# Performance work log

Measured on AMD Instinct MI355X. Metric: run time of the kernel, lower is better.

## Reference

```python
import jax, jax.numpy as jnp
import numpy as np

N_EMBEDS = 1024
N_HEADS = 16
HEAD_DIM = N_EMBEDS // N_HEADS
SCALE = HEAD_DIM ** (-0.5)
B, T = 2, 2048


def setup_inputs() -> dict:
    key = jax.random.key(0)
    k1, k2, k3, k4 = jax.random.split(key, 4)
    x = jax.random.normal(k1, (B, T, N_EMBEDS), dtype=jnp.float32)
    # Glorot-uniform-style init like keras Dense defaults (scale irrelevant for correctness)
    w_qkv = jax.random.normal(k2, (N_EMBEDS, 3 * N_EMBEDS), dtype=jnp.float32) * (N_EMBEDS ** -0.5)
    w_proj = jax.random.normal(k3, (N_EMBEDS, N_EMBEDS), dtype=jnp.float32) * (N_EMBEDS ** -0.5)
    b_proj = jnp.zeros((N_EMBEDS,), dtype=jnp.float32)
    return {"x": x, "w_qkv": w_qkv, "w_proj": w_proj, "b_proj": b_proj}


def reference(x, w_qkv, w_proj, b_proj):
    Bc, Tc, D = x.shape
    qkv = x @ w_qkv                                   # [B,T,3D]
    q, k, v = jnp.split(qkv, 3, axis=-1)
    def heads(t):
        return t.reshape(Bc, Tc, N_HEADS, HEAD_DIM).transpose(0, 2, 1, 3)  # [B,H,T,hd]
    q, k, v = heads(q), heads(k), heads(v)
    att = jnp.einsum("bhqd,bhkd->bhqk", q, k) * SCALE  # [B,H,T,T]
    causal = jnp.tril(jnp.ones((Tc, Tc), dtype=bool))[None, None]
    att = jnp.where(causal, att, jnp.float32(-1e9))
    att = jax.nn.softmax(att, axis=-1)
    out = jnp.einsum("bhqk,bhkd->bhqd", att, v)        # [B,H,T,hd]
    out = out.transpose(0, 2, 1, 3).reshape(Bc, Tc, D)
    return out @ w_proj + b_proj
```

## Files before the change

kernel.cpp:

```cpp
#include <hip/hip_runtime.h>
#include <hip/hip_bf16.h>


typedef __bf16 bf16;
typedef float f32x4 __attribute__((ext_vector_type(4)));
typedef float f32x16 __attribute__((ext_vector_type(16)));
typedef bf16 bf16x4 __attribute__((ext_vector_type(4)));
typedef bf16 bf16x8 __attribute__((ext_vector_type(8)));

#define B_ 2
#define T_ 2048
#define D_ 1024
#define H_ 16
#define HD_ 64
#define QSPLIT 9

__device__ __forceinline__ f32x16 mfma32(bf16x8 a, bf16x8 b, f32x16 c) {
    return __builtin_amdgcn_mfma_f32_32x32x16_bf16(a, b, c, 0, 0, 0);
}

__device__ __forceinline__ void gload16(void* l, const void* g) {
    __builtin_amdgcn_global_load_lds(
        (const __attribute__((address_space(1))) unsigned int*)g,
        (__attribute__((address_space(3))) unsigned int*)l, 16, 0, 0);
}

__device__ __forceinline__ f32x16 z16() {
    f32x16 v;
#pragma unroll
    for (int i = 0; i < 16; ++i) v[i] = 0.f;
    return v;
}

__global__ __launch_bounds__(256) void prep(
    const float* __restrict__ x, bf16* __restrict__ xb,
    const float* __restrict__ wqkv, bf16* __restrict__ wqkvt,
    const float* __restrict__ wproj, bf16* __restrict__ wprojt) {
    __shared__ float tile[32][33];
    const int bid = blockIdx.x;
    const int tid = threadIdx.x;
    if (bid < 4096) {
        int i = bid * 256 + tid;
        float4 v = ((const float4*)x)[i];
        bf16x4 o = { (bf16)v.x, (bf16)v.y, (bf16)v.z, (bf16)v.w };
        ((bf16x4*)xb)[i] = o;
        return;
    }
    const float* in;
    bf16* outp;
    int C, bx, by;
    if (bid < 4096 + 3072) {
        int r = bid - 4096;
        in = wqkv; outp = wqkvt; C = 3 * D_; bx = r % 96; by = r / 96;
    } else {
        int r = bid - 7168;
        in = wproj; outp = wprojt; C = D_; bx = r % 32; by = r / 32;
    }
    const int R = D_;
    const int tx = tid & 31, ty = tid >> 5;
    int cx = bx * 32 + tx;
    int r0 = by * 32;
#pragma unroll
    for (int j = 0; j < 32; j += 8)
        tile[ty + j][tx] = in[(size_t)(r0 + ty + j) * C + cx];
    __syncthreads();
    int rx = r0 + tx;
    int c0 = bx * 32;
#pragma unroll
    for (int j = 0; j < 32; j += 8)
        outp[(size_t)(c0 + ty + j) * R + rx] = (bf16)tile[tx][ty + j];
}

template <int MW, int NWN, int EPI>
__global__ __launch_bounds__(256) void gemm_k(
    const bf16* __restrict__ A, const bf16* __restrict__ Bt,
    int M, int N, int K,
    bf16* __restrict__ qb, bf16* __restrict__ kb, bf16* __restrict__ vt,
    const float* __restrict__ bias, float* __restrict__ outf) {
    constexpr int BM = 64 * MW;
    constexpr int BN = 64 * NWN;
    __shared__ bf16 sA[BM * 64];
    __shared__ bf16 sB[BN * 64];
    const int tid = threadIdx.x;
    const int wave = tid >> 6, lane = tid & 63;
    const int ln = lane & 31, hi = lane >> 5;
    const int wr = (wave >> 1) * (32 * MW);
    const int wc = (wave & 1) * (32 * NWN);
    const int m0 = blockIdx.x * BM, n0 = blockIdx.y * BN;

    f32x16 acc[MW][NWN];
#pragma unroll
    for (int mi = 0; mi < MW; ++mi)
#pragma unroll
        for (int ni = 0; ni < NWN; ++ni) acc[mi][ni] = z16();

    for (int k0 = 0; k0 < K; k0 += 64) {
        __syncthreads();
#pragma unroll
        for (int j = 0; j < 2 * MW; ++j) {
            int c = tid + 256 * j;
            int r = c >> 3, g = (c & 7) ^ (r & 7);
            gload16(&sA[c * 8], A + (size_t)(m0 + r) * K + k0 + 8 * g);
        }
#pragma unroll
        for (int j = 0; j < 2 * NWN; ++j) {
            int c = tid + 256 * j;
            int r = c >> 3, g = (c & 7) ^ (r & 7);
            gload16(&sB[c * 8], Bt + (size_t)(n0 + r) * K + k0 + 8 * g);
        }
        __syncthreads();
#pragma unroll
        for (int s = 0; s < 4; ++s) {
            bf16x8 av[MW], bv[NWN];
#pragma unroll
            for (int mi = 0; mi < MW; ++mi) {
                int r = wr + mi * 32 + ln;
                av[mi] = *(const bf16x8*)((const char*)sA + r * 128 +
                                          ((((s << 1) | hi) ^ (r & 7)) << 4));
            }
#pragma unroll
            for (int ni = 0; ni < NWN; ++ni) {
                int r = wc + ni * 32 + ln;
                bv[ni] = *(const bf16x8*)((const char*)sB + r * 128 +
                                          ((((s << 1) | hi) ^ (r & 7)) << 4));
            }
#pragma unroll
            for (int mi = 0; mi < MW; ++mi)
#pragma unroll
                for (int ni = 0; ni < NWN; ++ni)
                    acc[mi][ni] = mfma32(av[mi], bv[ni], acc[mi][ni]);
        }
    }

#pragma unroll
    for (int mi = 0; mi < MW; ++mi)
#pragma unroll
        for (int ni = 0; ni < NWN; ++ni) {
            int col = n0 + wc + ni * 32 + ln;
            if (EPI == 0) {
                int part = col >> 10, h = (col >> 6) & 15, d = col & 63;
                if (part == 2) {
#pragma unroll
                    for (int g4 = 0; g4 < 4; ++g4) {
                        int row = m0 + wr + mi * 32 + 8 * g4 + 4 * hi;
                        int bb = row >> 11, tt = row & (T_ - 1);
                        bf16x4 w;
#pragma unroll
                        for (int j = 0; j < 4; ++j)
                            w[j] = (bf16)acc[mi][ni][4 * g4 + j];
                        *(bf16x4*)&vt[(((size_t)(bb * H_ + h) * HD_) + d) * T_ + tt] = w;
                    }
                } else {
                    bf16* dst = (part == 0) ? qb : kb;
#pragma unroll
                    for (int r = 0; r < 16; ++r) {
                        int row = m0 + wr + mi * 32 + (r & 3) + 8 * (r >> 2) + 4 * hi;
                        int bb = row >> 11, tt = row & (T_ - 1);
                        dst[((size_t)(bb * H_ + h) * T_ + tt) * HD_ + d] =
                            (bf16)acc[mi][ni][r];
                    }
                }
            } else {
#pragma unroll
                for (int r = 0; r < 16; ++r) {
                    int row = m0 + wr + mi * 32 + (r & 3) + 8 * (r >> 2) + 4 * hi;
                    outf[(size_t)row * N + col] = acc[mi][ni][r] + bias[col];
                }
            }
        }
}

static __device__ const signed char QT_T[23] = {
    8, 7, 15, 15, 14, 14, 6, 13, 10, 10, 5, 11, 11, 12, 12, 13,
    0, 1, 2, 3, 4, 9, 9};
static __device__ const signed char SEG_T[23] = {
    -1, -1, 0, 1, 0, 1, -1, 0, 0, 1, -1, 0, 1, 0, 1, 1,
    -1, -1, -1, -1, -1, 0, 1};

__device__ __forceinline__ bf16x8 kread(const char* base, int row, int s, int hi) {
    int b = (row * 128 + s * 32 + hi * 16) ^ ((row & 7) << 4);
    return *(const bf16x8*)(base + b);
}
__device__ __forceinline__ bf16x8 vread(const char* base, int row, int s, int hi) {
    int sw = (row & 7) << 4;
    int b0 = (row * 128 + s * 32 + hi * 8) ^ sw;
    int b1 = (row * 128 + s * 32 + hi * 8 + 16) ^ sw;
    bf16x4 lo = *(const bf16x4*)(base + b0);
    bf16x4 hi4 = *(const bf16x4*)(base + b1);
    return __builtin_shufflevector(lo, hi4, 0, 1, 2, 3, 4, 5, 6, 7);
}

__global__ __launch_bounds__(256, 3) void attn_kernel(
    const bf16* __restrict__ qb, const bf16* __restrict__ kb,
    const bf16* __restrict__ vtb, bf16* __restrict__ ob,
    bf16* __restrict__ oP, float2* __restrict__ mlP) {
    __shared__ bf16 sK2[2][4096];
    __shared__ bf16 sV2[2][4096];

    const int bid = blockIdx.x;
    const int bh = bid & 31;
    const int sid = bid >> 5;
    const int qt = QT_T[sid];
    const int seg = SEG_T[sid];
    int t0, t1;
    if (seg < 0)       { t0 = 0;      t1 = 2 * qt + 2; }
    else if (seg == 0) { t0 = 0;      t1 = qt + 1; }
    else               { t0 = qt + 1; t1 = 2 * qt + 2; }
    const int b = bh >> 4, h = bh & 15;
    const int tid = threadIdx.x, wave = tid >> 6, lane = tid & 63;
    const int ln = lane & 31, hi = lane >> 5;
    const int qs = qt * 128 + wave * 32;
    const int qrow = qs + ln;

    const bf16* Qg = qb + (size_t)bh * (T_ * HD_);
    const bf16* Kg = kb + (size_t)bh * (T_ * HD_);
    const bf16* Vtg = vtb + (size_t)bh * (HD_ * T_);

    bf16x8 qf[4];
#pragma unroll
    for (int s = 0; s < 4; ++s) {
        bf16x8 v = *(const bf16x8*)&Qg[(size_t)qrow * HD_ + s * 16 + hi * 8];
#pragma unroll
        for (int e = 0; e < 8; ++e) v[e] = (bf16)((float)v[e] * 0.1803368801f);
        qf[s] = v;
    }
    bf16x8 ones;
#pragma unroll
    for (int e = 0; e < 8; ++e) ones[e] = (bf16)1.0f;

    const int rr0 = tid >> 3;
    const int gg = ((tid & 7) ^ (rr0 & 7)) * 8;

    {
        int kv0 = t0 * 64;
        gload16(&sK2[0][tid * 8], Kg + (size_t)(kv0 + rr0) * HD_ + gg);
        gload16(&sK2[0][(tid + 256) * 8], Kg + (size_t)(kv0 + rr0 + 32) * HD_ + gg);
        gload16(&sV2[0][tid * 8], Vtg + (size_t)rr0 * T_ + kv0 + gg);
        gload16(&sV2[0][(tid + 256) * 8], Vtg + (size_t)(rr0 + 32) * T_ + kv0 + gg);
    }
    __syncthreads();

    const float NINF = -__builtin_inff();
    f32x16 oA = z16(), oB = z16();
    float mR = NINF, lR = 0.f;
    int cur = 0;

    for (int t = t0; t < t1; ++t) {
        if ((t + 1) < t1) {
            int kv0 = (t + 1) * 64;
            bf16* kd = sK2[cur ^ 1];
            bf16* vd = sV2[cur ^ 1];
            gload16(&kd[tid * 8], Kg + (size_t)(kv0 + rr0) * HD_ + gg);
            gload16(&kd[(tid + 256) * 8], Kg + (size_t)(kv0 + rr0 + 32) * HD_ + gg);
            gload16(&vd[tid * 8], Vtg + (size_t)rr0 * T_ + kv0 + gg);
            gload16(&vd[(tid + 256) * 8], Vtg + (size_t)(rr0 + 32) * T_ + kv0 + gg);
        }

        if (64 * t <= qs + 31) {
            const char* kbase = (const char*)sK2[cur];
            const char* vbase = (const char*)sV2[cur];

            f32x16 p0 = z16(), p1 = z16();
            __builtin_amdgcn_s_setprio(1);
#pragma unroll
            for (int s = 0; s < 4; ++s) {
                bf16x8 a0 = kread(kbase, ln, s, hi);
                bf16x8 a1 = kread(kbase, ln + 32, s, hi);
                p0 = mfma32(a0, qf[s], p0);
                p1 = mfma32(a1, qf[s], p1);
            }
            __builtin_amdgcn_s_setprio(0);

            if (64 * t + 63 > qs) {
                int kvb = 64 * t + 4 * hi;
#pragma unroll
                for (int r = 0; r < 16; ++r) {
                    int kvr = kvb + (r & 3) + 8 * (r >> 2);
                    if (kvr > qrow) p0[r] = NINF;
                    if (kvr + 32 > qrow) p1[r] = NINF;
                }
            }

            float mx0 = NINF, mx1 = NINF, mx2 = NINF, mx3 = NINF;
#pragma unroll
            for (int r = 0; r < 16; r += 4) {
                mx0 = fmaxf(fmaxf(p0[r], p1[r]), mx0);
                mx1 = fmaxf(fmaxf(p0[r + 1], p1[r + 1]), mx1);
                mx2 = fmaxf(fmaxf(p0[r + 2], p1[r + 2]), mx2);
                mx3 = fmaxf(fmaxf(p0[r + 3], p1[r + 3]), mx3);
            }
            float pm = fmaxf(fmaxf(mx0, mx1), fmaxf(mx2, mx3));
            pm = fmaxf(pm, __shfl_xor(pm, 32));

            if (__any(pm > mR + 8.f)) {
                float mnew = fmaxf(mR, pm);
                float fac = exp2f(mR - mnew);
                lR *= fac;
#pragma unroll
                for (int r = 0; r < 16; ++r) { oA[r] *= fac; oB[r] *= fac; }
                mR = mnew;
            }

            bf16x8 pa0, pa1, pa2, pa3;
#pragma unroll
            for (int e = 0; e < 8; ++e) {
                pa0[e] = (bf16)exp2f(p0[e] - mR);
                pa1[e] = (bf16)exp2f(p0[8 + e] - mR);
                pa2[e] = (bf16)exp2f(p1[e] - mR);
                pa3[e] = (bf16)exp2f(p1[8 + e] - mR);
            }

            __builtin_amdgcn_s_setprio(1);
            f32x16 sacc = mfma32(ones, pa0, z16());
            sacc = mfma32(ones, pa1, sacc);
            sacc = mfma32(ones, pa2, sacc);
            sacc = mfma32(ones, pa3, sacc);
#pragma unroll
            for (int s = 0; s < 4; ++s) {
                bf16x8 pas = (s == 0) ? pa0 : (s == 1) ? pa1 : (s == 2) ? pa2 : pa3;
                oA = mfma32(vread(vbase, ln, s, hi), pas, oA);
                oB = mfma32(vread(vbase, ln + 32, s, hi), pas, oB);
            }
            __builtin_amdgcn_s_setprio(0);
            lR += sacc[0];
        }

        __syncthreads();
        cur ^= 1;
    }

    if (seg < 0) {
        float inv = 1.f / lR;
        bf16* orow = ob + ((size_t)(b * T_ + qrow)) * D_ + h * HD_;
#pragma unroll
        for (int g = 0; g < 4; ++g) {
            bf16x4 w, w2;
#pragma unroll
            for (int j = 0; j < 4; ++j) {
                w[j] = (bf16)(oA[4 * g + j] * inv);
                w2[j] = (bf16)(oB[4 * g + j] * inv);
            }
            *(bf16x4*)&orow[4 * hi + 8 * g] = w;
            *(bf16x4*)&orow[32 + 4 * hi + 8 * g] = w2;
        }
    } else {
        int row = wave * 32 + ln;
        bf16* prow;
        if (seg == 0) {
            prow = ob + ((size_t)(b * T_ + qrow)) * D_ + h * HD_;
        } else {
            size_t sbase = (size_t)bh * (16 - QSPLIT) + (qt - QSPLIT);
            prow = oP + (sbase * 128 + row) * 64;
        }
#pragma unroll
        for (int g = 0; g < 4; ++g) {
            bf16x4 w, w2;
#pragma unroll
            for (int j = 0; j < 4; ++j) {
                w[j] = (bf16)oA[4 * g + j];
                w2[j] = (bf16)oB[4 * g + j];
            }
            *(bf16x4*)&prow[4 * hi + 8 * g] = w;
            *(bf16x4*)&prow[32 + 4 * hi + 8 * g] = w2;
        }
        if (hi == 0)
            mlP[(((size_t)bh * (16 - QSPLIT) + (qt - QSPLIT)) * 2 + seg) * 128 + row] =
                make_float2(mR, lR);
    }
}

__global__ __launch_bounds__(256) void attn_merge(
    const bf16* __restrict__ oP, const float2* __restrict__ mlP,
    bf16* __restrict__ ob) {
    constexpr int NQS = 16 - QSPLIT;
    int gid = blockIdx.x * 256 + threadIdx.x;
    int bh = gid / (NQS * 128);
    int rem = gid - bh * (NQS * 128);
    int qi = rem >> 7, row = rem & 127;
    int b = bh >> 4, h = bh & 15;
    int t = (QSPLIT + qi) * 128 + row;
    size_t sbase = (size_t)bh * NQS + qi;
    float2 ml0 = mlP[(sbase * 2 + 0) * 128 + row];
    float2 ml1 = mlP[(sbase * 2 + 1) * 128 + row];
    float ms = fmaxf(ml0.x, ml1.x);
    float w0 = exp2f(ml0.x - ms), w1 = exp2f(ml1.x - ms);
    float inv = 1.f / (ml0.y * w0 + ml1.y * w1);
    w0 *= inv; w1 *= inv;
    bf16* dst = ob + ((size_t)(b * T_ + t)) * D_ + h * HD_;
    const bf16* r1 = oP + (sbase * 128 + row) * 64;
#pragma unroll
    for (int g = 0; g < 8; ++g) {
        bf16x8 a = *(const bf16x8*)&dst[g * 8];
        bf16x8 c = *(const bf16x8*)&r1[g * 8];
        bf16x8 o;
#pragma unroll
        for (int j = 0; j < 8; ++j)
            o[j] = (bf16)((float)a[j] * w0 + (float)c[j] * w1);
        *(bf16x8*)&dst[g * 8] = o;
    }
}

extern "C" void kernel_launch(void* const* d_in, const int* in_sizes, int n_in,
                              void* d_out, int out_size, void* d_ws, size_t ws_size,
                              hipStream_t stream) {
    const float* x = (const float*)d_in[0];
    const float* w_qkv = (const float*)d_in[1];
    const float* w_proj = (const float*)d_in[2];
    const float* b_proj = (const float*)d_in[3];
    float* out = (float*)d_out;
    char* ws = (char*)d_ws;

    bf16* xb = (bf16*)(ws);
    bf16* ob = (bf16*)(ws);
    bf16* wqkvt = (bf16*)(ws + 8388608);
    bf16* oP = (bf16*)(ws + 8388608);
    float2* mlP = (float2*)(ws + 12058624);
    bf16* wprojt = (bf16*)(ws + 14680064);
    bf16* qbuf = (bf16*)(ws + 16777216);
    bf16* kbuf = (bf16*)(ws + 25165824);
    bf16* vtbuf = (bf16*)(ws + 33554432);

    prep<<<8192, 256, 0, stream>>>(x, xb, w_qkv, wqkvt, w_proj, wprojt);

    gemm_k<2, 2, 0><<<dim3((B_ * T_) / 128, (3 * D_) / 128), 256, 0, stream>>>(
        xb, wqkvt, B_ * T_, 3 * D_, D_, qbuf, kbuf, vtbuf, nullptr, nullptr);

    attn_kernel<<<23 * 32, 256, 0, stream>>>(qbuf, kbuf, vtbuf, ob, oP, mlP);
    attn_merge<<<112, 256, 0, stream>>>(oP, mlP, ob);

    gemm_k<1, 2, 1><<<dim3((B_ * T_) / 64, D_ / 128), 256, 0, stream>>>(
        ob, wprojt, B_ * T_, D_, D_, nullptr, nullptr, nullptr, b_proj, out);
}
```

Before: 110.6 us.

## Use 256-row query tiles with 512 threads and up-to-3-way KV split

The attention kernel moves from 128-row query tiles with 256 threads to 256-row tiles with 512 threads (8 waves), so each staged K/V tile is shared by more query rows. A new static schedule splits long causal strips into 2 or 3 KV segments, and the merge kernel combines up to three partials. The w_proj transpose moves from the prep kernel into spare blocks of the merge launch, and workspace buffers are re-laid out to alias the freed K buffer. The aim is more K/V reuse and better load balance across CUs, at the cost of fewer, larger blocks and a more intricate merge.

```diff
diff --git a/kernel.cpp b/kernel.cpp
--- a/kernel.cpp
+++ b/kernel.cpp
@@ -13,7 +13,8 @@
 #define D_ 1024
 #define H_ 16
 #define HD_ 64
-#define QSPLIT 9
+#define SEGS_PER_BH 15
+#define PSLOTS 7
 
 __device__ __forceinline__ f32x16 mfma32(bf16x8 a, bf16x8 b, f32x16 c) {
     return __builtin_amdgcn_mfma_f32_32x32x16_bf16(a, b, c, 0, 0, 0);
@@ -34,8 +35,7 @@
 
 __global__ __launch_bounds__(256) void prep(
     const float* __restrict__ x, bf16* __restrict__ xb,
-    const float* __restrict__ wqkv, bf16* __restrict__ wqkvt,
-    const float* __restrict__ wproj, bf16* __restrict__ wprojt) {
+    const float* __restrict__ wqkv, bf16* __restrict__ wqkvt) {
     __shared__ float tile[32][33];
     const int bid = blockIdx.x;
     const int tid = threadIdx.x;
@@ -46,29 +46,21 @@
         ((bf16x4*)xb)[i] = o;
         return;
     }
-    const float* in;
-    bf16* outp;
-    int C, bx, by;
-    if (bid < 4096 + 3072) {
-        int r = bid - 4096;
-        in = wqkv; outp = wqkvt; C = 3 * D_; bx = r % 96; by = r / 96;
-    } else {
-        int r = bid - 7168;
-        in = wproj; outp = wprojt; C = D_; bx = r % 32; by = r / 32;
-    }
-    const int R = D_;
+    int r = bid - 4096;
+    const int C = 3 * D_;
+    int bx = r % 96, by = r / 96;
     const int tx = tid & 31, ty = tid >> 5;
     int cx = bx * 32 + tx;
     int r0 = by * 32;
 #pragma unroll
     for (int j = 0; j < 32; j += 8)
-        tile[ty + j][tx] = in[(size_t)(r0 + ty + j) * C + cx];
+        tile[ty + j][tx] = wqkv[(size_t)(r0 + ty + j) * C + cx];
     __syncthreads();
     int rx = r0 + tx;
     int c0 = bx * 32;
 #pragma unroll
     for (int j = 0; j < 32; j += 8)
-        outp[(size_t)(c0 + ty + j) * R + rx] = (bf16)tile[tx][ty + j];
+        wqkvt[(size_t)(c0 + ty + j) * D_ + rx] = (bf16)tile[tx][ty + j];
 }
 
 template <int MW, int NWN, int EPI>
@@ -170,12 +162,14 @@
         }
 }
 
-static __device__ const signed char QT_T[23] = {
-    8, 7, 15, 15, 14, 14, 6, 13, 10, 10, 5, 11, 11, 12, 12, 13,
-    0, 1, 2, 3, 4, 9, 9};
-static __device__ const signed char SEG_T[23] = {
-    -1, -1, 0, 1, 0, 1, -1, 0, 0, 1, -1, 0, 1, 0, 1, 1,
-    -1, -1, -1, -1, -1, 0, 1};
+static __device__ const signed char QT_T[SEGS_PER_BH] =
+    {5, 5, 2, 7, 7, 7, 6, 6, 4, 4, 6, 3, 3, 1, 0};
+static __device__ const signed char SEG_T[SEGS_PER_BH] =
+    {0, 1, -1, 0, 1, 2, 0, 1, 0, 1, 2, 0, 1, -1, -1};
+static __device__ const signed char NS_T[SEGS_PER_BH] =
+    {2, 2, 1, 3, 3, 3, 3, 3, 2, 2, 3, 2, 2, 1, 1};
+static __device__ const signed char PSLOT_T[SEGS_PER_BH] =
+    {0, 2, 0, 0, 5, 6, 0, 3, 0, 1, 4, 0, 0, 0, 0};
 
 __device__ __forceinline__ bf16x8 kread(const char* base, int row, int s, int hi) {
     int b = (row * 128 + s * 32 + hi * 16) ^ ((row & 7) << 4);
@@ -190,7 +184,7 @@
     return __builtin_shufflevector(lo, hi4, 0, 1, 2, 3, 4, 5, 6, 7);
 }
 
-__global__ __launch_bounds__(256, 3) void attn_kernel(
+__global__ __launch_bounds__(512, 4) void attn_kernel(
     const bf16* __restrict__ qb, const bf16* __restrict__ kb,
     const bf16* __restrict__ vtb, bf16* __restrict__ ob,
     bf16* __restrict__ oP, float2* __restrict__ mlP) {
@@ -202,14 +196,19 @@
     const int sid = bid >> 5;
     const int qt = QT_T[sid];
     const int seg = SEG_T[sid];
+    const int ns = NS_T[sid];
+    const int nt = 4 * qt + 4;
     int t0, t1;
-    if (seg < 0)       { t0 = 0;      t1 = 2 * qt + 2; }
-    else if (seg == 0) { t0 = 0;      t1 = qt + 1; }
-    else               { t0 = qt + 1; t1 = 2 * qt + 2; }
+    if (seg < 0) { t0 = 0; t1 = nt; }
+    else {
+        int len = (nt + ns - 1) / ns;
+        t0 = seg * len;
+        t1 = (t0 + len < nt) ? t0 + len : nt;
+    }
     const int b = bh >> 4, h = bh & 15;
     const int tid = threadIdx.x, wave = tid >> 6, lane = tid & 63;
     const int ln = lane & 31, hi = lane >> 5;
-    const int qs = qt * 128 + wave * 32;
+    const int qs = qt * 256 + wave * 32;
     const int qrow = qs + ln;
 
     const bf16* Qg = qb + (size_t)bh * (T_ * HD_);
@@ -234,9 +233,7 @@
     {
         int kv0 = t0 * 64;
         gload16(&sK2[0][tid * 8], Kg + (size_t)(kv0 + rr0) * HD_ + gg);
-        gload16(&sK2[0][(tid + 256) * 8], Kg + (size_t)(kv0 + rr0 + 32) * HD_ + gg);
         gload16(&sV2[0][tid * 8], Vtg + (size_t)rr0 * T_ + kv0 + gg);
-        gload16(&sV2[0][(tid + 256) * 8], Vtg + (size_t)(rr0 + 32) * T_ + kv0 + gg);
     }
     __syncthreads();
 
@@ -248,12 +245,8 @@
     for (int t = t0; t < t1; ++t) {
         if ((t + 1) < t1) {
             int kv0 = (t + 1) * 64;
-            bf16* kd = sK2[cur ^ 1];
-            bf16* vd = sV2[cur ^ 1];
-            gload16(&kd[tid * 8], Kg + (size_t)(kv0 + rr0) * HD_ + gg);
-            gload16(&kd[(tid + 256) * 8], Kg + (size_t)(kv0 + rr0 + 32) * HD_ + gg);
-            gload16(&vd[tid * 8], Vtg + (size_t)rr0 * T_ + kv0 + gg);
-            gload16(&vd[(tid + 256) * 8], Vtg + (size_t)(rr0 + 32) * T_ + kv0 + gg);
+            gload16(&sK2[cur ^ 1][tid * 8], Kg + (size_t)(kv0 + rr0) * HD_ + gg);
+            gload16(&sV2[cur ^ 1][tid * 8], Vtg + (size_t)rr0 * T_ + kv0 + gg);
         }
 
         if (64 * t <= qs + 31) {
@@ -349,8 +342,7 @@
         if (seg == 0) {
             prow = ob + ((size_t)(b * T_ + qrow)) * D_ + h * HD_;
         } else {
-            size_t sbase = (size_t)bh * (16 - QSPLIT) + (qt - QSPLIT);
-            prow = oP + (sbase * 128 + row) * 64;
+            prow = oP + (((size_t)bh * PSLOTS + PSLOT_T[sid]) * 256 + row) * 64;
         }
 #pragma unroll
         for (int g = 0; g < 4; ++g) {
@@ -364,38 +356,73 @@
             *(bf16x4*)&prow[32 + 4 * hi + 8 * g] = w2;
         }
         if (hi == 0)
-            mlP[(((size_t)bh * (16 - QSPLIT) + (qt - QSPLIT)) * 2 + seg) * 128 + row] =
+            mlP[(((size_t)bh * 5 + (qt - 3)) * 3 + seg) * 256 + row] =
                 make_float2(mR, lR);
     }
 }
 
 __global__ __launch_bounds__(256) void attn_merge(
     const bf16* __restrict__ oP, const float2* __restrict__ mlP,
-    bf16* __restrict__ ob) {
-    constexpr int NQS = 16 - QSPLIT;
-    int gid = blockIdx.x * 256 + threadIdx.x;
-    int bh = gid / (NQS * 128);
-    int rem = gid - bh * (NQS * 128);
-    int qi = rem >> 7, row = rem & 127;
+    bf16* __restrict__ ob,
+    const float* __restrict__ wproj, bf16* __restrict__ wprojt) {
+    __shared__ float tile[32][33];
+    const int bid = blockIdx.x;
+    const int tid = threadIdx.x;
+    if (bid >= 160) {
+        int r = bid - 160;
+        int bx = r & 31, by = r >> 5;
+        const int tx = tid & 31, ty = tid >> 5;
+        int cx = bx * 32 + tx;
+        int r0 = by * 32;
+#pragma unroll
+        for (int j = 0; j < 32; j += 8)
+            tile[ty + j][tx] = wproj[(size_t)(r0 + ty + j) * D_ + cx];
+        __syncthreads();
+        int rx = r0 + tx;
+        int c0 = bx * 32;
+#pragma unroll
+        for (int j = 0; j < 32; j += 8)
+            wprojt[(size_t)(c0 + ty + j) * D_ + rx] = (bf16)tile[tx][ty + j];
+        return;
+    }
+    int gid = bid * 256 + tid;
+    int bh = gid / (5 * 256);
+    int rem = gid - bh * (5 * 256);
+    int strip = rem >> 8, row = rem & 255;
+    int qt = strip + 3;
+    int ns = (strip < 3) ? 2 : 3;
     int b = bh >> 4, h = bh & 15;
-    int t = (QSPLIT + qi) * 128 + row;
-    size_t sbase = (size_t)bh * NQS + qi;
-    float2 ml0 = mlP[(sbase * 2 + 0) * 128 + row];
-    float2 ml1 = mlP[(sbase * 2 + 1) * 128 + row];
-    float ms = fmaxf(ml0.x, ml1.x);
-    float w0 = exp2f(ml0.x - ms), w1 = exp2f(ml1.x - ms);
-    float inv = 1.f / (ml0.y * w0 + ml1.y * w1);
-    w0 *= inv; w1 *= inv;
+    int t = qt * 256 + row;
+    int s1 = (strip < 3) ? strip : (strip == 3 ? 3 : 5);
+
+    size_t mlb = ((size_t)bh * 5 + strip) * 3;
+    float2 ml0 = mlP[(mlb + 0) * 256 + row];
+    float2 ml1 = mlP[(mlb + 1) * 256 + row];
+    float2 ml2 = (ns == 3) ? mlP[(mlb + 2) * 256 + row] : make_float2(-1e30f, 0.f);
+    float ms = fmaxf(fmaxf(ml0.x, ml1.x), ml2.x);
+    float w0 = exp2f(ml0.x - ms), w1 = exp2f(ml1.x - ms), w2 = exp2f(ml2.x - ms);
+    if (ns < 3) w2 = 0.f;
+    float inv = 1.f / (ml0.y * w0 + ml1.y * w1 + ml2.y * w2);
+    w0 *= inv; w1 *= inv; w2 *= inv;
+
     bf16* dst = ob + ((size_t)(b * T_ + t)) * D_ + h * HD_;
-    const bf16* r1 = oP + (sbase * 128 + row) * 64;
+    const bf16* r1 = oP + (((size_t)bh * PSLOTS + s1) * 256 + row) * 64;
+    const bf16* r2 = oP + (((size_t)bh * PSLOTS + s1 + 1) * 256 + row) * 64;
 #pragma unroll
     for (int g = 0; g < 8; ++g) {
         bf16x8 a = *(const bf16x8*)&dst[g * 8];
         bf16x8 c = *(const bf16x8*)&r1[g * 8];
         bf16x8 o;
-#pragma unroll
-        for (int j = 0; j < 8; ++j)
-            o[j] = (bf16)((float)a[j] * w0 + (float)c[j] * w1);
+        if (ns == 3) {
+            bf16x8 d2 = *(const bf16x8*)&r2[g * 8];
+#pragma unroll
+            for (int j = 0; j < 8; ++j)
+                o[j] = (bf16)((float)a[j] * w0 + (float)c[j] * w1 + (float)d2[j] * w2);
+        } else {
+#pragma unroll
+            for (int j = 0; j < 8; ++j)
+                o[j] = (bf16)((float)a[j] * w0 + (float)c[j] * w1);
+        }
         *(bf16x8*)&dst[g * 8] = o;
     }
 }
@@ -414,19 +441,20 @@
     bf16* ob = (bf16*)(ws);
     bf16* wqkvt = (bf16*)(ws + 8388608);
     bf16* oP = (bf16*)(ws + 8388608);
-    float2* mlP = (float2*)(ws + 12058624);
-    bf16* wprojt = (bf16*)(ws + 14680064);
+    float2* mlP = (float2*)(ws + 15728640);
     bf16* qbuf = (bf16*)(ws + 16777216);
     bf16* kbuf = (bf16*)(ws + 25165824);
+    bf16* wprojt = (bf16*)(ws + 25165824);
     bf16* vtbuf = (bf16*)(ws + 33554432);
 
-    prep<<<8192, 256, 0, stream>>>(x, xb, w_qkv, wqkvt, w_proj, wprojt);
+    prep<<<7168, 256, 0, stream>>>(x, xb, w_qkv, wqkvt);
 
     gemm_k<2, 2, 0><<<dim3((B_ * T_) / 128, (3 * D_) / 128), 256, 0, stream>>>(
         xb, wqkvt, B_ * T_, 3 * D_, D_, qbuf, kbuf, vtbuf, nullptr, nullptr);
 
-    attn_kernel<<<23 * 32, 256, 0, stream>>>(qbuf, kbuf, vtbuf, ob, oP, mlP);
-    attn_merge<<<112, 256, 0, stream>>>(oP, mlP, ob);
+    attn_kernel<<<SEGS_PER_BH * 32, 512, 0, stream>>>(qbuf, kbuf, vtbuf, ob, oP, mlP);
+
+    attn_merge<<<1184, 256, 0, stream>>>(oP, mlP, ob, w_proj, wprojt);
 
     gemm_k<1, 2, 1><<<dim3((B_ * T_) / 64, D_ / 128), 256, 0, stream>>>(
         ob, wprojt, B_ * T_, D_, D_, nullptr, nullptr, nullptr, b_proj, out);
```

Result: slower. 117.2 us (+5.9%).
